# Optimization experiments

Measured on AMD Instinct MI355X. Metric: run time of the kernel, lower is better.

The kernel has to match this reference:

```python
import jax, jax.numpy as jnp
import numpy as np

N = 100000        # nodes
E = 1600000       # edges (avg degree 16)
F_IN = 512        # num_features
H1, D1 = 8, 8     # layer-1 heads x per-head dim (concat -> 64)
C = 16            # num_classes (layer-2: 1 head, dim C)
NEG_SLOPE = 0.2


def setup_inputs() -> dict:
    key = jax.random.key(0)
    ks = jax.random.split(key, 8)
    x = jax.random.normal(ks[0], (N, F_IN), dtype=jnp.float32)
    edge_index = jax.random.randint(ks[1], (2, E), 0, N, dtype=jnp.int64)
    W1 = jax.random.normal(ks[2], (F_IN, H1 * D1), dtype=jnp.float32) / np.float32(np.sqrt(F_IN))
    a1_src = jax.random.normal(ks[3], (H1, D1), dtype=jnp.float32) * 0.1
    a1_dst = jax.random.normal(ks[4], (H1, D1), dtype=jnp.float32) * 0.1
    W2 = jax.random.normal(ks[5], (H1 * D1, C), dtype=jnp.float32) / np.float32(np.sqrt(H1 * D1))
    a2_src = jax.random.normal(ks[6], (1, C), dtype=jnp.float32) * 0.1
    a2_dst = jax.random.normal(ks[7], (1, C), dtype=jnp.float32) * 0.1
    return {"x": x, "edge_index": edge_index, "W1": W1, "a1_src": a1_src,
            "a1_dst": a1_dst, "W2": W2, "a2_src": a2_src, "a2_dst": a2_dst}


def gat_layer(x, src, dst, W, a_s, a_d, heads, out_dim):
    """Multi-head GAT conv: gather -> per-edge leaky-relu score -> segment
    softmax over destination -> scatter-aggregate. Returns [N, heads, out_dim]."""
    n = x.shape[0]
    h = (x @ W).reshape(n, heads, out_dim)            # [N, H, D]
    es = jnp.einsum('nhd,hd->nh', h, a_s)             # source attention term
    ed = jnp.einsum('nhd,hd->nh', h, a_d)             # dest attention term
    e = jax.nn.leaky_relu(es[src] + ed[dst], NEG_SLOPE)   # [E, H]
    m = jax.ops.segment_max(e, dst, num_segments=n)       # stable softmax max
    ex = jnp.exp(e - m[dst])
    s = jax.ops.segment_sum(ex, dst, num_segments=n)
    alpha = ex / s[dst]                               # [E, H]
    out = jax.ops.segment_sum(h[src] * alpha[..., None], dst, num_segments=n)
    return out                                        # [N, H, D]


def reference(x, edge_index, W1, a1_src, a1_dst, W2, a2_src, a2_dst):
    n = x.shape[0]
    loop = jnp.arange(n, dtype=edge_index.dtype)
    src = jnp.concatenate([edge_index[0], loop])      # add self-loops
    dst = jnp.concatenate([edge_index[1], loop])
    # eval mode: dropout(p=0.6, training=False) is identity
    h1 = gat_layer(x, src, dst, W1, a1_src, a1_dst, H1, D1).reshape(n, H1 * D1)
    h1 = jax.nn.elu(h1)
    h2 = gat_layer(h1, src, dst, W2, a2_src, a2_dst, 1, C).reshape(n, C)
    return jax.nn.log_softmax(h2, axis=1)
```

## Files before the change

kernel.cpp:

```cpp
#include <hip/hip_runtime.h>
#include <hip/hip_bf16.h>

#define F_IN 512
#define H1 8
#define D1 8
#define F_MID 64
#define C 16
#define NEG_SLOPE 0.2f
#define BIN_CHUNK 4096
#define NB_MAX 1024
#define BUCKET_SHIFT 7
#define BUCKET_STRIDE 3072
#define SRC_BITS 17
#define SRC_MASK ((1 << SRC_BITS) - 1)

typedef __attribute__((ext_vector_type(8))) short bf16x8;
typedef __attribute__((ext_vector_type(4))) float f32x4;

static __device__ __forceinline__ unsigned short f2bf(float f) {
    __hip_bfloat16 h = __float2bfloat16(f);
    return *(unsigned short*)&h;
}

__global__ __launch_bounds__(256) void k_bin(const int* __restrict__ src,
                                             const int* __restrict__ dst,
                                             int* __restrict__ gcur,
                                             int* __restrict__ bucketed,
                                             int n_edges, int nb) {
    __shared__ int cnt[NB_MAX];
    __shared__ int base[NB_MAX];
    const int t = threadIdx.x;
    const int eb = blockIdx.x * BIN_CHUNK;
    for (int b = t; b < nb; b += 256) cnt[b] = 0;
    __syncthreads();
#pragma unroll
    for (int i = 0; i < BIN_CHUNK / 256; ++i) {
        int e = eb + i * 256 + t;
        if (e < n_edges) atomicAdd(&cnt[dst[e] >> BUCKET_SHIFT], 1);
    }
    __syncthreads();
    for (int b = t; b < nb; b += 256) {
        int c = cnt[b];
        base[b] = c > 0 ? atomicAdd(&gcur[b], c) : 0;
        cnt[b] = 0;
    }
    __syncthreads();
#pragma unroll
    for (int i = 0; i < BIN_CHUNK / 256; ++i) {
        int e = eb + i * 256 + t;
        if (e < n_edges) {
            int d = dst[e];
            int b = d >> BUCKET_SHIFT;
            int local = atomicAdd(&cnt[b], 1);
            bucketed[(size_t)b * BUCKET_STRIDE + base[b] + local] =
                ((d & ((1 << BUCKET_SHIFT) - 1)) << SRC_BITS) | src[e];
        }
    }
}

__global__ __launch_bounds__(256) void k_place(const int* __restrict__ gcur,
                                               const int* __restrict__ bucketed,
                                               int* __restrict__ row_start,
                                               int* __restrict__ sorted_src,
                                               int n_nodes, int n_edges) {
    __shared__ int stage[BUCKET_STRIDE];
    __shared__ int cnt[1 << BUCKET_SHIFT];
    __shared__ int cur[1 << BUCKET_SHIFT];
    __shared__ int wsum[4];
    const int t = threadIdx.x;
    const int b = blockIdx.x;
    if (t < (1 << BUCKET_SHIFT)) cnt[t] = 0;
    int pre = 0;
    for (int j = t; j < b; j += 256) pre += gcur[j];
#pragma unroll
    for (int off = 1; off < 64; off <<= 1) pre += __shfl_xor(pre, off, 64);
    if ((t & 63) == 0) wsum[t >> 6] = pre;
    __syncthreads();
    const int base0 = wsum[0] + wsum[1] + wsum[2] + wsum[3];
    if (b == 0 && t == 0) row_start[n_nodes] = n_edges;

    const int total = gcur[b];
    const int* bp = bucketed + (size_t)b * BUCKET_STRIDE;
    for (int i = t; i < total; i += 256) {
        int e = bp[i];
        stage[i] = e;
        atomicAdd(&cnt[e >> SRC_BITS], 1);
    }
    __syncthreads();
    if (t < (1 << BUCKET_SHIFT)) cur[t] = cnt[t];
    __syncthreads();
#pragma unroll
    for (int d = 1; d < (1 << BUCKET_SHIFT); d <<= 1) {
        int u = 0;
        if (t < (1 << BUCKET_SHIFT) && t >= d) u = cur[t - d];
        __syncthreads();
        if (t < (1 << BUCKET_SHIFT)) cur[t] += u;
        __syncthreads();
    }
    if (t < (1 << BUCKET_SHIFT)) {
        int node = (b << BUCKET_SHIFT) + t;
        int excl = cur[t] - cnt[t];
        if (node < n_nodes) row_start[node] = base0 + excl;
        cur[t] = excl;
    }
    __syncthreads();
    for (int i = t; i < total; i += 256) {
        int e = stage[i];
        int p = atomicAdd(&cur[e >> SRC_BITS], 1);
        sorted_src[base0 + p] = e & SRC_MASK;
    }
}

__global__ __launch_bounds__(256) void k_w1t(const float* __restrict__ W1,
                                             __hip_bfloat16* __restrict__ w1t) {
    int idx = blockIdx.x * 256 + threadIdx.x;
    int k = idx >> 6, n = idx & 63;
    w1t[n * F_IN + k] = __float2bfloat16(W1[idx]);
}

__global__ __launch_bounds__(256) void k_gemm1(const float* __restrict__ x,
                                               const __hip_bfloat16* __restrict__ w1t,
                                               const float* __restrict__ a1s,
                                               const float* __restrict__ a1d,
                                               __hip_bfloat16* __restrict__ h1b,
                                               float* __restrict__ es1,
                                               float* __restrict__ ed1, int n_nodes) {
    __shared__ unsigned short Xs[64][72];
    __shared__ unsigned short Ws[64][72];
    __shared__ float sas[64], sad[64];
    const int t = threadIdx.x;
    if (t < 64) sas[t] = a1s[t];
    else if (t < 128) sad[t - 64] = a1d[t - 64];

    const int wv = t >> 6, l = t & 63;
    const int q = l >> 4, m16 = l & 15;
    const int rowbase = blockIdx.x * 64;

    const int sr = t >> 2, sf = t & 3;
    int gx = rowbase + sr;
    gx = gx < n_nodes ? gx : n_nodes - 1;
    const float* xrow = x + (size_t)gx * F_IN;
    const __hip_bfloat16* wrow = w1t + (size_t)sr * F_IN;

    f32x4 acc[4];
#pragma unroll
    for (int i = 0; i < 4; ++i) acc[i] = (f32x4){0.f, 0.f, 0.f, 0.f};

    for (int kt = 0; kt < F_IN; kt += 64) {
#pragma unroll
        for (int j = 0; j < 4; ++j) {
            float4 v = *(const float4*)(xrow + kt + sf * 16 + j * 4);
            ushort4 b;
            b.x = f2bf(v.x); b.y = f2bf(v.y); b.z = f2bf(v.z); b.w = f2bf(v.w);
            *(ushort4*)&Xs[sr][sf * 16 + j * 4] = b;
        }
#pragma unroll
        for (int j = 0; j < 2; ++j) {
            *(int4*)&Ws[sr][sf * 16 + j * 8] =
                *(const int4*)(wrow + kt + sf * 16 + j * 8);
        }
        __syncthreads();
#pragma unroll
        for (int kk = 0; kk < 2; ++kk) {
            bf16x8 bfrag = *(const bf16x8*)&Xs[wv * 16 + m16][kk * 32 + q * 8];
#pragma unroll
            for (int tn = 0; tn < 4; ++tn) {
                bf16x8 afrag = *(const bf16x8*)&Ws[tn * 16 + m16][kk * 32 + q * 8];
                acc[tn] = __builtin_amdgcn_mfma_f32_16x16x32_bf16(afrag, bfrag, acc[tn], 0, 0, 0);
            }
        }
        __syncthreads();
    }

    const int node = rowbase + wv * 16 + m16;
    const bool ok = node < n_nodes;
#pragma unroll
    for (int tn = 0; tn < 4; ++tn) {
        const f32x4 a = acc[tn];
        const int nw0 = tn * 16 + q * 4;
        float vs = a.x * sas[nw0] + a.y * sas[nw0 + 1] + a.z * sas[nw0 + 2] + a.w * sas[nw0 + 3];
        float vd = a.x * sad[nw0] + a.y * sad[nw0 + 1] + a.z * sad[nw0 + 2] + a.w * sad[nw0 + 3];
        vs += __shfl_xor(vs, 16, 64);
        vd += __shfl_xor(vd, 16, 64);
        if (ok) {
            ushort4 b;
            b.x = f2bf(a.x); b.y = f2bf(a.y); b.z = f2bf(a.z); b.w = f2bf(a.w);
            *(ushort4*)(h1b + (size_t)node * F_MID + nw0) = b;
            if ((q & 1) == 0) {
                const int head = 2 * tn + (q >> 1);
                es1[node * H1 + head] = vs;
                ed1[node * H1 + head] = vd;
            }
        }
    }
}

__global__ __launch_bounds__(256) void k_gather1(const int* __restrict__ row_start,
                                                 const int* __restrict__ sorted_src,
                                                 const __hip_bfloat16* __restrict__ h1b,
                                                 const float* __restrict__ es1,
                                                 const float* __restrict__ ed1,
                                                 float* __restrict__ h1, int n_nodes) {
    const int n = blockIdx.x * 4 + (threadIdx.x >> 6);
    if (n >= n_nodes) return;
    const int lane = threadIdx.x & 63;
    const int h = lane >> 3;
    const float edh = ed1[n * H1 + h];
    const int beg = row_start[n], end = row_start[n + 1];
    float acc = 0.f, den = 0.f;
    for (int base = beg; base < end; base += 64) {
        const int m = min(64, end - base);
        const int li = lane < m ? lane : (m - 1);
        const int myS = sorted_src[base + li];
        int j = 0;
        for (; j + 4 <= m; j += 4) {
            const int s0 = __shfl(myS, j, 64), s1 = __shfl(myS, j + 1, 64);
            const int s2 = __shfl(myS, j + 2, 64), s3 = __shfl(myS, j + 3, 64);
            float e0 = es1[s0 * H1 + h], e1 = es1[s1 * H1 + h];
            float e2 = es1[s2 * H1 + h], e3 = es1[s3 * H1 + h];
            const float f0 = __bfloat162float(h1b[(size_t)s0 * F_MID + lane]);
            const float f1 = __bfloat162float(h1b[(size_t)s1 * F_MID + lane]);
            const float f2 = __bfloat162float(h1b[(size_t)s2 * F_MID + lane]);
            const float f3 = __bfloat162float(h1b[(size_t)s3 * F_MID + lane]);
            e0 += edh; e1 += edh; e2 += edh; e3 += edh;
            e0 = e0 > 0.f ? e0 : NEG_SLOPE * e0;
            e1 = e1 > 0.f ? e1 : NEG_SLOPE * e1;
            e2 = e2 > 0.f ? e2 : NEG_SLOPE * e2;
            e3 = e3 > 0.f ? e3 : NEG_SLOPE * e3;
            const float w0 = __expf(e0), w1 = __expf(e1), w2 = __expf(e2), w3 = __expf(e3);
            acc += w0 * f0 + w1 * f1 + w2 * f2 + w3 * f3;
            den += (w0 + w1) + (w2 + w3);
        }
        for (; j < m; ++j) {
            const int s = __shfl(myS, j, 64);
            float ev = es1[s * H1 + h] + edh;
            ev = ev > 0.f ? ev : NEG_SLOPE * ev;
            const float w = __expf(ev);
            acc += w * __bfloat162float(h1b[(size_t)s * F_MID + lane]);
            den += w;
        }
    }
    float evs = es1[n * H1 + h] + edh;
    evs = evs > 0.f ? evs : NEG_SLOPE * evs;
    const float ws = __expf(evs);
    acc += ws * __bfloat162float(h1b[(size_t)n * F_MID + lane]);
    den += ws;
    float v = acc / den;
    v = v > 0.f ? v : expm1f(v);
    h1[(size_t)n * F_MID + lane] = v;
}

__global__ void k_gemm2(const float* __restrict__ h1, const float* __restrict__ W2,
                        const float* __restrict__ a2s, const float* __restrict__ a2d,
                        __hip_bfloat16* __restrict__ h2b, float* __restrict__ es2,
                        float* __restrict__ ed2, int n_nodes) {
    __shared__ float w2s[F_MID * C];
    __shared__ float h1s[16][F_MID + 1];
    const int t = threadIdx.x;
    const int nb = blockIdx.x * 16;
    for (int i = t; i < F_MID * C; i += 256) w2s[i] = W2[i];
    for (int i = t; i < 16 * F_MID; i += 256) {
        int r = i >> 6, k = i & 63;
        int n = nb + r;
        h1s[r][k] = h1[(size_t)(n < n_nodes ? n : n_nodes - 1) * F_MID + k];
    }
    __syncthreads();
    const int r = t >> 4, c = t & 15;
    const int n = nb + r;
    float acc = 0.f;
#pragma unroll
    for (int k = 0; k < F_MID; ++k) acc += h1s[r][k] * w2s[k * C + c];
    float vs = acc * a2s[c], vd = acc * a2d[c];
#pragma unroll
    for (int off = 1; off < 16; off <<= 1) {
        vs += __shfl_xor(vs, off, 64);
        vd += __shfl_xor(vd, off, 64);
    }
    if (n < n_nodes) {
        h2b[(size_t)n * C + c] = __float2bfloat16(acc);
        if (c == 0) { es2[n] = vs; ed2[n] = vd; }
    }
}

__global__ __launch_bounds__(256) void k_gather2(const int* __restrict__ row_start,
                                                 const int* __restrict__ sorted_src,
                                                 const __hip_bfloat16* __restrict__ h2b,
                                                 const float* __restrict__ es2,
                                                 const float* __restrict__ ed2,
                                                 float* __restrict__ out, int n_nodes) {
    const int n = blockIdx.x * 16 + (threadIdx.x >> 4);
    if (n >= n_nodes) return;
    const int lane = threadIdx.x & 63;
    const int c = lane & 15;
    const int g = lane >> 4;
    const float ed = ed2[n];
    const int beg = row_start[n], end = row_start[n + 1];
    float acc = 0.f, den = 0.f;
    for (int base = beg; base < end; base += 16) {
        const int m = min(16, end - base);
        const int li = c < m ? c : (m - 1);
        const int myS = sorted_src[base + li];
        int j = 0;
        for (; j + 4 <= m; j += 4) {
            const int s0 = __shfl(myS, g * 16 + j, 64), s1 = __shfl(myS, g * 16 + j + 1, 64);
            const int s2 = __shfl(myS, g * 16 + j + 2, 64), s3 = __shfl(myS, g * 16 + j + 3, 64);
            float e0 = es2[s0] + ed, e1 = es2[s1] + ed, e2 = es2[s2] + ed, e3 = es2[s3] + ed;
            const float f0 = __bfloat162float(h2b[(size_t)s0 * C + c]);
            const float f1 = __bfloat162float(h2b[(size_t)s1 * C + c]);
            const float f2 = __bfloat162float(h2b[(size_t)s2 * C + c]);
            const float f3 = __bfloat162float(h2b[(size_t)s3 * C + c]);
            e0 = e0 > 0.f ? e0 : NEG_SLOPE * e0;
            e1 = e1 > 0.f ? e1 : NEG_SLOPE * e1;
            e2 = e2 > 0.f ? e2 : NEG_SLOPE * e2;
            e3 = e3 > 0.f ? e3 : NEG_SLOPE * e3;
            const float w0 = __expf(e0), w1 = __expf(e1), w2 = __expf(e2), w3 = __expf(e3);
            acc += w0 * f0 + w1 * f1 + w2 * f2 + w3 * f3;
            den += (w0 + w1) + (w2 + w3);
        }
        for (; j < m; ++j) {
            const int s = __shfl(myS, g * 16 + j, 64);
            float ev = es2[s] + ed;
            ev = ev > 0.f ? ev : NEG_SLOPE * ev;
            const float w = __expf(ev);
            acc += w * __bfloat162float(h2b[(size_t)s * C + c]);
            den += w;
        }
    }
    float evs = es2[n] + ed;
    evs = evs > 0.f ? evs : NEG_SLOPE * evs;
    const float ws = __expf(evs);
    acc += ws * __bfloat162float(h2b[(size_t)n * C + c]);
    den += ws;
    const float v = acc / den;
    float mx = v;
#pragma unroll
    for (int off = 1; off < 16; off <<= 1) mx = fmaxf(mx, __shfl_xor(mx, off, 64));
    float se = __expf(v - mx);
#pragma unroll
    for (int off = 1; off < 16; off <<= 1) se += __shfl_xor(se, off, 64);
    out[(size_t)n * C + c] = v - mx - __logf(se);
}

extern "C" void kernel_launch(void* const* d_in, const int* in_sizes, int n_in,
                              void* d_out, int out_size, void* d_ws, size_t ws_size,
                              hipStream_t stream) {
    const float* x   = (const float*)d_in[0];
    const int*   ei  = (const int*)d_in[1];
    const float* W1  = (const float*)d_in[2];
    const float* a1s = (const float*)d_in[3];
    const float* a1d = (const float*)d_in[4];
    const float* W2  = (const float*)d_in[5];
    const float* a2s = (const float*)d_in[6];
    const float* a2d = (const float*)d_in[7];
    float* out = (float*)d_out;

    const int n_nodes = in_sizes[0] / F_IN;
    const int n_edges = in_sizes[1] / 2;
    const int* src = ei;
    const int* dst = ei + n_edges;
    const int nb = (n_nodes + (1 << BUCKET_SHIFT) - 1) >> BUCKET_SHIFT;

    float* fws = (float*)d_ws;
    float* es1 = fws;
    float* ed1 = es1 + (size_t)n_nodes * H1;
    float* h1  = ed1 + (size_t)n_nodes * H1;
    float* es2 = h1  + (size_t)n_nodes * F_MID;
    float* ed2 = es2 + n_nodes;
    __hip_bfloat16* h1b = (__hip_bfloat16*)(ed2 + n_nodes);
    __hip_bfloat16* h2b = h1b + (size_t)n_nodes * F_MID;
    __hip_bfloat16* w1t = h2b + (size_t)n_nodes * C;
    int* iws         = (int*)(w1t + F_IN * F_MID);
    int* gcur        = iws;
    int* row_start   = gcur + NB_MAX;
    int* sorted_src  = row_start + n_nodes + 1;
    int* bucketed    = sorted_src + n_edges;

    hipMemsetAsync(gcur, 0, NB_MAX * sizeof(int), stream);

    k_bin<<<(n_edges + BIN_CHUNK - 1) / BIN_CHUNK, 256, 0, stream>>>(src, dst, gcur, bucketed, n_edges, nb);
    k_place<<<nb, 256, 0, stream>>>(gcur, bucketed, row_start, sorted_src, n_nodes, n_edges);

    k_w1t<<<(F_IN * F_MID) / 256, 256, 0, stream>>>(W1, w1t);
    k_gemm1<<<(n_nodes + 63) / 64, 256, 0, stream>>>(x, w1t, a1s, a1d, h1b, es1, ed1, n_nodes);
    k_gather1<<<(n_nodes + 3) / 4, 256, 0, stream>>>(row_start, sorted_src, h1b, es1, ed1, h1, n_nodes);

    k_gemm2<<<(n_nodes + 15) / 16, 256, 0, stream>>>(h1, W2, a2s, a2d, h2b, es2, ed2, n_nodes);
    k_gather2<<<(n_nodes + 15) / 16, 256, 0, stream>>>(row_start, sorted_src, h2b, es2, ed2, out, n_nodes);
}
```

Baseline: 482.1 us.

## Fuse W1 transpose into binning, read W1 from global, store h1 as bf16

Several independent changes. The W1 transpose/convert kernel is merged into the edge-binning launch as extra blocks, which saves one launch. k_bin now keeps dst values in registers so it does not read them twice. gemm1 drops the shared-memory W tile and loads weight fragments straight from global or L2, and the layer-1 output h1 is stored as bf16 instead of fp32, halving the bytes gemm2 has to read. Reading fragments from global adds load latency inside the MFMA loop, and the bf16 intermediate lowers precision.

Result: no change. 478.5 us (-0.7%).

```diff
diff --git a/kernel.cpp b/kernel.cpp
--- a/kernel.cpp
+++ b/kernel.cpp
@@ -22,22 +22,34 @@
     return *(unsigned short*)&h;
 }
 
-__global__ __launch_bounds__(256) void k_bin(const int* __restrict__ src,
-                                             const int* __restrict__ dst,
-                                             int* __restrict__ gcur,
-                                             int* __restrict__ bucketed,
-                                             int n_edges, int nb) {
+__global__ __launch_bounds__(256) void k_bin_w1t(const int* __restrict__ src,
+                                                 const int* __restrict__ dst,
+                                                 int* __restrict__ gcur,
+                                                 int* __restrict__ bucketed,
+                                                 const float* __restrict__ W1,
+                                                 __hip_bfloat16* __restrict__ w1t,
+                                                 int n_edges, int nb, int nbin) {
+    const int t = threadIdx.x;
+    if ((int)blockIdx.x >= nbin) {
+        int idx = ((int)blockIdx.x - nbin) * 256 + t;
+        int k = idx >> 6, n = idx & 63;
+        w1t[n * F_IN + k] = __float2bfloat16(W1[idx]);
+        return;
+    }
     __shared__ int cnt[NB_MAX];
     __shared__ int base[NB_MAX];
-    const int t = threadIdx.x;
     const int eb = blockIdx.x * BIN_CHUNK;
-    for (int b = t; b < nb; b += 256) cnt[b] = 0;
-    __syncthreads();
+    int dc[BIN_CHUNK / 256];
 #pragma unroll
     for (int i = 0; i < BIN_CHUNK / 256; ++i) {
         int e = eb + i * 256 + t;
-        if (e < n_edges) atomicAdd(&cnt[dst[e] >> BUCKET_SHIFT], 1);
-    }
+        dc[i] = (e < n_edges) ? dst[e] : -1;
+    }
+    for (int b = t; b < nb; b += 256) cnt[b] = 0;
+    __syncthreads();
+#pragma unroll
+    for (int i = 0; i < BIN_CHUNK / 256; ++i)
+        if (dc[i] >= 0) atomicAdd(&cnt[dc[i] >> BUCKET_SHIFT], 1);
     __syncthreads();
     for (int b = t; b < nb; b += 256) {
         int c = cnt[b];
@@ -47,9 +59,9 @@
     __syncthreads();
 #pragma unroll
     for (int i = 0; i < BIN_CHUNK / 256; ++i) {
-        int e = eb + i * 256 + t;
-        if (e < n_edges) {
-            int d = dst[e];
+        if (dc[i] >= 0) {
+            int e = eb + i * 256 + t;
+            int d = dc[i];
             int b = d >> BUCKET_SHIFT;
             int local = atomicAdd(&cnt[b], 1);
             bucketed[(size_t)b * BUCKET_STRIDE + base[b] + local] =
@@ -111,13 +123,6 @@
     }
 }
 
-__global__ __launch_bounds__(256) void k_w1t(const float* __restrict__ W1,
-                                             __hip_bfloat16* __restrict__ w1t) {
-    int idx = blockIdx.x * 256 + threadIdx.x;
-    int k = idx >> 6, n = idx & 63;
-    w1t[n * F_IN + k] = __float2bfloat16(W1[idx]);
-}
-
 __global__ __launch_bounds__(256) void k_gemm1(const float* __restrict__ x,
                                                const __hip_bfloat16* __restrict__ w1t,
                                                const float* __restrict__ a1s,
@@ -126,7 +131,6 @@
                                                float* __restrict__ es1,
                                                float* __restrict__ ed1, int n_nodes) {
     __shared__ unsigned short Xs[64][72];
-    __shared__ unsigned short Ws[64][72];
     __shared__ float sas[64], sad[64];
     const int t = threadIdx.x;
     if (t < 64) sas[t] = a1s[t];
@@ -140,7 +144,6 @@
     int gx = rowbase + sr;
     gx = gx < n_nodes ? gx : n_nodes - 1;
     const float* xrow = x + (size_t)gx * F_IN;
-    const __hip_bfloat16* wrow = w1t + (size_t)sr * F_IN;
 
     f32x4 acc[4];
 #pragma unroll
@@ -154,18 +157,14 @@
             b.x = f2bf(v.x); b.y = f2bf(v.y); b.z = f2bf(v.z); b.w = f2bf(v.w);
             *(ushort4*)&Xs[sr][sf * 16 + j * 4] = b;
         }
-#pragma unroll
-        for (int j = 0; j < 2; ++j) {
-            *(int4*)&Ws[sr][sf * 16 + j * 8] =
-                *(const int4*)(wrow + kt + sf * 16 + j * 8);
-        }
         __syncthreads();
 #pragma unroll
         for (int kk = 0; kk < 2; ++kk) {
             bf16x8 bfrag = *(const bf16x8*)&Xs[wv * 16 + m16][kk * 32 + q * 8];
 #pragma unroll
             for (int tn = 0; tn < 4; ++tn) {
-                bf16x8 afrag = *(const bf16x8*)&Ws[tn * 16 + m16][kk * 32 + q * 8];
+                bf16x8 afrag = *(const bf16x8*)(w1t + (size_t)(tn * 16 + m16) * F_IN
+                                                + kt + kk * 32 + q * 8);
                 acc[tn] = __builtin_amdgcn_mfma_f32_16x16x32_bf16(afrag, bfrag, acc[tn], 0, 0, 0);
             }
         }
@@ -200,7 +199,7 @@
                                                  const __hip_bfloat16* __restrict__ h1b,
                                                  const float* __restrict__ es1,
                                                  const float* __restrict__ ed1,
-                                                 float* __restrict__ h1, int n_nodes) {
+                                                 __hip_bfloat16* __restrict__ h1c, int n_nodes) {
     const int n = blockIdx.x * 4 + (threadIdx.x >> 6);
     if (n >= n_nodes) return;
     const int lane = threadIdx.x & 63;
@@ -247,10 +246,10 @@
     den += ws;
     float v = acc / den;
     v = v > 0.f ? v : expm1f(v);
-    h1[(size_t)n * F_MID + lane] = v;
-}
-
-__global__ void k_gemm2(const float* __restrict__ h1, const float* __restrict__ W2,
+    h1c[(size_t)n * F_MID + lane] = __float2bfloat16(v);
+}
+
+__global__ void k_gemm2(const __hip_bfloat16* __restrict__ h1c, const float* __restrict__ W2,
                         const float* __restrict__ a2s, const float* __restrict__ a2d,
                         __hip_bfloat16* __restrict__ h2b, float* __restrict__ es2,
                         float* __restrict__ ed2, int n_nodes) {
@@ -259,10 +258,15 @@
     const int t = threadIdx.x;
     const int nb = blockIdx.x * 16;
     for (int i = t; i < F_MID * C; i += 256) w2s[i] = W2[i];
-    for (int i = t; i < 16 * F_MID; i += 256) {
-        int r = i >> 6, k = i & 63;
+    {
+        int r = t >> 4, k4 = (t & 15) << 2;
         int n = nb + r;
-        h1s[r][k] = h1[(size_t)(n < n_nodes ? n : n_nodes - 1) * F_MID + k];
+        const __hip_bfloat16* p = h1c + (size_t)(n < n_nodes ? n : n_nodes - 1) * F_MID + k4;
+        ushort4 v = *(const ushort4*)p;
+        h1s[r][k4 + 0] = __bfloat162float(*(const __hip_bfloat16*)&v.x);
+        h1s[r][k4 + 1] = __bfloat162float(*(const __hip_bfloat16*)&v.y);
+        h1s[r][k4 + 2] = __bfloat162float(*(const __hip_bfloat16*)&v.z);
+        h1s[r][k4 + 3] = __bfloat162float(*(const __hip_bfloat16*)&v.w);
     }
     __syncthreads();
     const int r = t >> 4, c = t & 15;
@@ -359,16 +363,17 @@
     const int* src = ei;
     const int* dst = ei + n_edges;
     const int nb = (n_nodes + (1 << BUCKET_SHIFT) - 1) >> BUCKET_SHIFT;
+    const int nbin = (n_edges + BIN_CHUNK - 1) / BIN_CHUNK;
 
     float* fws = (float*)d_ws;
     float* es1 = fws;
     float* ed1 = es1 + (size_t)n_nodes * H1;
-    float* h1  = ed1 + (size_t)n_nodes * H1;
-    float* es2 = h1  + (size_t)n_nodes * F_MID;
+    float* es2 = ed1 + (size_t)n_nodes * H1;
     float* ed2 = es2 + n_nodes;
     __hip_bfloat16* h1b = (__hip_bfloat16*)(ed2 + n_nodes);
     __hip_bfloat16* h2b = h1b + (size_t)n_nodes * F_MID;
-    __hip_bfloat16* w1t = h2b + (size_t)n_nodes * C;
+    __hip_bfloat16* h1c = h2b + (size_t)n_nodes * C;
+    __hip_bfloat16* w1t = h1c + (size_t)n_nodes * F_MID;
     int* iws         = (int*)(w1t + F_IN * F_MID);
     int* gcur        = iws;
     int* row_start   = gcur + NB_MAX;
@@ -377,13 +382,13 @@
 
     hipMemsetAsync(gcur, 0, NB_MAX * sizeof(int), stream);
 
-    k_bin<<<(n_edges + BIN_CHUNK - 1) / BIN_CHUNK, 256, 0, stream>>>(src, dst, gcur, bucketed, n_edges, nb);
+    k_bin_w1t<<<nbin + (F_IN * F_MID) / 256, 256, 0, stream>>>(src, dst, gcur, bucketed,
+                                                               W1, w1t, n_edges, nb, nbin);
     k_place<<<nb, 256, 0, stream>>>(gcur, bucketed, row_start, sorted_src, n_nodes, n_edges);
 
-    k_w1t<<<(F_IN * F_MID) / 256, 256, 0, stream>>>(W1, w1t);
     k_gemm1<<<(n_nodes + 63) / 64, 256, 0, stream>>>(x, w1t, a1s, a1d, h1b, es1, ed1, n_nodes);
-    k_gather1<<<(n_nodes + 3) / 4, 256, 0, stream>>>(row_start, sorted_src, h1b, es1, ed1, h1, n_nodes);
-
-    k_gemm2<<<(n_nodes + 15) / 16, 256, 0, stream>>>(h1, W2, a2s, a2d, h2b, es2, ed2, n_nodes);
+    k_gather1<<<(n_nodes + 3) / 4, 256, 0, stream>>>(row_start, sorted_src, h1b, es1, ed1, h1c, n_nodes);
+
+    k_gemm2<<<(n_nodes + 15) / 16, 256, 0, stream>>>(h1c, W2, a2s, a2d, h2b, es2, ed2, n_nodes);
     k_gather2<<<(n_nodes + 15) / 16, 256, 0, stream>>>(row_start, sorted_src, h2b, es2, ed2, out, n_nodes);
 }
```
